# Kernel optimization log

Hardware: AMD Instinct MI355X
Metric: run time of the kernel (lower is better)

The kernel has to match this reference:

```python
import jax, jax.numpy as jnp
import numpy as np

EPS = 1e-5
INV_SQRT2 = 0.7071067811865476

def _rmsnorm(x, w):
    rms = jnp.sqrt(jnp.sum(x * x, axis=-1) / x.shape[-1] + EPS)
    return x / rms[..., None] * w

def _gelu(x):
    # exact erf-based GELU as in the torch module
    return x * (1.0 + jax.scipy.special.erf(x * INV_SQRT2)) * 0.5

def setup_inputs() -> dict:
    key = jax.random.key(0)
    ks = jax.random.split(key, 8)
    B, S, D, DFF = 4, 2048, 1024, 4096
    s = 0.02  # realistic init scale keeps softmax non-degenerate
    return {
        "x": jax.random.normal(ks[0], (B, S, D), jnp.float32),
        "ln1": jax.random.uniform(ks[1], (D,), jnp.float32),
        "ln2": jax.random.uniform(ks[2], (D,), jnp.float32),
        "ffn1": jax.random.normal(ks[3], (DFF, D), jnp.float32) * s,
        "ffn2": jax.random.normal(ks[4], (D, DFF), jnp.float32) * s,
        "k_proj": jax.random.normal(ks[5], (D, D), jnp.float32) * s,
        "q_proj": jax.random.normal(ks[6], (D, D), jnp.float32) * s,
        "v_proj": jax.random.normal(ks[7], (D, D), jnp.float32) * s,
        "out_proj": jax.random.normal(jax.random.fold_in(key, 99), (D, D), jnp.float32) * s,
    }

def reference(x, ln1, ln2, ffn1, ffn2, k_proj, q_proj, v_proj, out_proj):
    S = x.shape[1]
    d_k = x.shape[-1]
    # --- attention branch (single-head, as in source) ---
    h = _rmsnorm(x, ln1)
    Q = h @ q_proj.T  # [B,S,D]
    K = h @ k_proj.T
    V = h @ v_proj.T
    scores = jnp.einsum('bqd,bkd->bqk', Q, K) / jnp.sqrt(jnp.float32(d_k))
    attn = jax.nn.softmax(scores, axis=-1)
    # source: softmax first, then zero out strict-upper (future) entries, renormalize
    causal = jnp.tril(jnp.ones((S, S), jnp.float32))
    attn = attn * causal
    attn = attn / jnp.sum(attn, axis=-1, keepdims=True)
    mh = jnp.einsum('bqk,bkd->bqd', attn, V) @ out_proj
    y = x + mh
    # --- FFN branch: NOTE source feeds RMSNorm2(x), not y ---
    h2 = _rmsnorm(x, ln2)
    ff = _gelu(h2 @ ffn1.T) @ ffn2.T
    return y + ff
```

## Files before the change

### kernel.cpp

```cpp
#include <hip/hip_runtime.h>
#include <math.h>

typedef __bf16 bf16_t;
typedef __bf16 bf16x8 __attribute__((ext_vector_type(8)));
typedef float f32x4 __attribute__((ext_vector_type(4)));

#define LDS16(g, l) __builtin_amdgcn_global_load_lds( \
    (__attribute__((address_space(1))) void*)(g),     \
    (__attribute__((address_space(3))) void*)(l), 16, 0, 0)

__global__ __launch_bounds__(256) void prep_kernel(
    const float* __restrict__ qp, const float* __restrict__ kp,
    const float* __restrict__ vp, const float* __restrict__ f1,
    const float* __restrict__ f2, const float* __restrict__ op,
    const float* __restrict__ x, const float* __restrict__ ln1,
    bf16_t* __restrict__ qkvb, bf16_t* __restrict__ f1b,
    bf16_t* __restrict__ f2b, bf16_t* __restrict__ opT,
    bf16_t* __restrict__ h1)
{
    __shared__ float tile[32][33];
    __shared__ float red[4];
    int bid = blockIdx.x;
    int t = threadIdx.x;
    if (bid < 11264) {
        size_t i = ((size_t)bid * 256 + t) * 4;
        const float* src;
        bf16_t* dst;
        if (i < 3145728) {
            if (i < 1048576)      { src = qp + i;             dst = qkvb + i; }
            else if (i < 2097152) { src = kp + (i - 1048576); dst = qkvb + i; }
            else                  { src = vp + (i - 2097152); dst = qkvb + i; }
        } else if (i < 7340032) { src = f1 + (i - 3145728); dst = f1b + (i - 3145728); }
        else                    { src = f2 + (i - 7340032); dst = f2b + (i - 7340032); }
        float4 v = *(const float4*)src;
        dst[0] = (bf16_t)v.x; dst[1] = (bf16_t)v.y;
        dst[2] = (bf16_t)v.z; dst[3] = (bf16_t)v.w;
    } else if (bid < 12288) {
        int b2 = bid - 11264;
        int c0 = (b2 & 31) * 32, r0 = (b2 >> 5) * 32;
        int tx = t & 31, ty = t >> 5;
#pragma unroll
        for (int i = 0; i < 32; i += 8)
            tile[ty + i][tx] = op[(size_t)(r0 + ty + i) * 1024 + c0 + tx];
        __syncthreads();
#pragma unroll
        for (int i = 0; i < 32; i += 8)
            opT[(size_t)(c0 + ty + i) * 1024 + r0 + tx] = (bf16_t)tile[tx][ty + i];
    } else {
        int row = bid - 12288;
        float4 xv = ((const float4*)(x + (size_t)row * 1024))[t];
        float ss = xv.x * xv.x + xv.y * xv.y + xv.z * xv.z + xv.w * xv.w;
#pragma unroll
        for (int o = 32; o > 0; o >>= 1) ss += __shfl_xor(ss, o, 64);
        if ((t & 63) == 0) red[t >> 6] = ss;
        __syncthreads();
        ss = red[0] + red[1] + red[2] + red[3];
        float rinv = rsqrtf(ss * (1.0f / 1024.0f) + 1e-5f);
        float4 wv = ((const float4*)ln1)[t];
        bf16_t* hp = h1 + (size_t)row * 1024 + t * 4;
        hp[0] = (bf16_t)(xv.x * rinv * wv.x);
        hp[1] = (bf16_t)(xv.y * rinv * wv.y);
        hp[2] = (bf16_t)(xv.z * rinv * wv.z);
        hp[3] = (bf16_t)(xv.w * rinv * wv.w);
    }
}

__global__ __launch_bounds__(256) void rmsnorm_kernel(
    const float* __restrict__ x, const float* __restrict__ w,
    bf16_t* __restrict__ h)
{
    int row = blockIdx.x;
    int t = threadIdx.x;
    float4 xv = ((const float4*)(x + (size_t)row * 1024))[t];
    float ss = xv.x * xv.x + xv.y * xv.y + xv.z * xv.z + xv.w * xv.w;
#pragma unroll
    for (int o = 32; o > 0; o >>= 1) ss += __shfl_xor(ss, o, 64);
    __shared__ float red[4];
    if ((t & 63) == 0) red[t >> 6] = ss;
    __syncthreads();
    ss = red[0] + red[1] + red[2] + red[3];
    float rinv = rsqrtf(ss * (1.0f / 1024.0f) + 1e-5f);
    float4 wv = ((const float4*)w)[t];
    bf16_t* hp = h + (size_t)row * 1024 + t * 4;
    hp[0] = (bf16_t)(xv.x * rinv * wv.x);
    hp[1] = (bf16_t)(xv.y * rinv * wv.y);
    hp[2] = (bf16_t)(xv.z * rinv * wv.z);
    hp[3] = (bf16_t)(xv.w * rinv * wv.w);
}

__global__ __launch_bounds__(256) void transpose_bf16(
    const bf16_t* __restrict__ in, bf16_t* __restrict__ out,
    int rows, int ldin, long long sIn, long long sOut)
{
    __shared__ bf16_t tile[32][33];
    int b = blockIdx.z;
    const bf16_t* ip = in + (long long)b * sIn;
    bf16_t* op = out + (long long)b * sOut;
    int c0 = blockIdx.x * 32, r0 = blockIdx.y * 32;
    int tx = threadIdx.x & 31, ty = threadIdx.x >> 5;
#pragma unroll
    for (int i = 0; i < 32; i += 8)
        tile[ty + i][tx] = ip[(size_t)(r0 + ty + i) * ldin + c0 + tx];
    __syncthreads();
#pragma unroll
    for (int i = 0; i < 32; i += 8)
        op[(size_t)(c0 + ty + i) * rows + r0 + tx] = tile[tx][ty + i];
}

__global__ __launch_bounds__(256) void causal_softmax_kernel(bf16_t* __restrict__ SP)
{
    const int S = 2048;
    int q = blockIdx.x, b = blockIdx.y;
    bf16_t* row = SP + ((size_t)b * S + q) * S;
    int t = threadIdx.x;
    int j0 = t * 8;
    int Jstore = ((q >> 7) + 1) << 7;

    float v[8];
    if (j0 + 7 <= q) {
        bf16x8 xv = *(const bf16x8*)(row + j0);
#pragma unroll
        for (int i = 0; i < 8; i++) v[i] = (float)xv[i];
    } else if (j0 <= q) {
#pragma unroll
        for (int i = 0; i < 8; i++)
            v[i] = (j0 + i <= q) ? (float)row[j0 + i] : -1e30f;
    } else {
#pragma unroll
        for (int i = 0; i < 8; i++) v[i] = -1e30f;
    }

    float mx = v[0];
#pragma unroll
    for (int i = 1; i < 8; i++) mx = fmaxf(mx, v[i]);
#pragma unroll
    for (int o = 32; o > 0; o >>= 1) mx = fmaxf(mx, __shfl_xor(mx, o, 64));
    __shared__ float sm[4], ssum[4];
    if ((t & 63) == 0) sm[t >> 6] = mx;
    __syncthreads();
    mx = fmaxf(fmaxf(sm[0], sm[1]), fmaxf(sm[2], sm[3]));

    float e[8];
    float sum = 0.f;
#pragma unroll
    for (int i = 0; i < 8; i++) {
        e[i] = (v[i] > -1e29f) ? expf(v[i] - mx) : 0.f;
        sum += e[i];
    }
#pragma unroll
    for (int o = 32; o > 0; o >>= 1) sum += __shfl_xor(sum, o, 64);
    if ((t & 63) == 0) ssum[t >> 6] = sum;
    __syncthreads();
    sum = ssum[0] + ssum[1] + ssum[2] + ssum[3];
    float r = 1.0f / sum;

    if (j0 < Jstore) {
        bf16x8 ov;
#pragma unroll
        for (int i = 0; i < 8; i++) ov[i] = (bf16_t)(e[i] * r);
        *(bf16x8*)(row + j0) = ov;
    }
}

template <int EPI, bool TRI, bool CKLOOP>
__global__ __launch_bounds__(256) void gemm_bt(
    const bf16_t* __restrict__ A, int lda, const bf16_t* __restrict__ B, int ldb,
    void* Cv, int ldc, const float* R,
    int K, int Nt, long long sA, long long sB, long long sC, float scale)
{
    int bz = blockIdx.z;
    int bm, bn;
    if (TRI) {
        int i = blockIdx.x;
        bm = (int)((sqrtf(8.0f * i + 1.0f) - 1.0f) * 0.5f);
        while ((bm + 1) * (bm + 2) / 2 <= i) bm++;
        while (bm * (bm + 1) / 2 > i) bm--;
        bn = i - bm * (bm + 1) / 2;
    } else {
        int id = blockIdx.x;
        int xcd = id & 7, p = id >> 3;
        int cn = Nt >> 3;
        bn = xcd * cn + p % cn;
        bm = p / cn;
    }

    __shared__ __align__(16) bf16_t At[128 * 64];
    __shared__ __align__(16) bf16_t Bt[128 * 64];
    int t = threadIdx.x;
    int w = t >> 6, l = t & 63;
    int wm = w >> 1, wn = w & 1;
    int lane_m = l & 15, quad = l >> 4;

    const bf16_t* Ag = A + (long long)bz * sA + (size_t)(bm * 128) * lda;
    const bf16_t* Bg = B + (long long)bz * sB + (size_t)(bn * 128) * ldb;

    int Keff = K;
    if (CKLOOP) {
        int kk = (bm + 1) * 128;
        if (kk < K) Keff = kk;
    }

    f32x4 acc[4][4] = {};

    int rb = w * 8 + (l >> 3);
    int g0 = ((l & 7) ^ ((l >> 3) & 7)) * 8;
    const bf16_t* a0[4];
    const bf16_t* b0[4];
#pragma unroll
    for (int j = 0; j < 4; j++) {
        size_t ro = (size_t)(rb + 32 * j);
        a0[j] = Ag + ro * lda + g0;
        b0[j] = Bg + ro * ldb + g0;
    }

    int s0 = (quad ^ (lane_m & 7)) * 8;
    int s1 = ((4 + quad) ^ (lane_m & 7)) * 8;

    for (int kt = 0; kt < Keff; kt += 64) {
        __syncthreads();
#pragma unroll
        for (int j = 0; j < 4; j++) {
            LDS16(a0[j] + kt, At + (size_t)w * 512 + j * 2048);
            LDS16(b0[j] + kt, Bt + (size_t)w * 512 + j * 2048);
        }
        __syncthreads();

#pragma unroll
        for (int h = 0; h < 2; h++) {
            int sh = h ? s1 : s0;
            bf16x8 af[4], bfr[4];
#pragma unroll
            for (int mi = 0; mi < 4; mi++)
                af[mi] = *(const bf16x8*)(At + (wm * 64 + mi * 16 + lane_m) * 64 + sh);
#pragma unroll
            for (int ni = 0; ni < 4; ni++)
                bfr[ni] = *(const bf16x8*)(Bt + (wn * 64 + ni * 16 + lane_m) * 64 + sh);
#pragma unroll
            for (int mi = 0; mi < 4; mi++)
#pragma unroll
                for (int ni = 0; ni < 4; ni++)
                    acc[mi][ni] = __builtin_amdgcn_mfma_f32_16x16x32_bf16(
                        af[mi], bfr[ni], acc[mi][ni], 0, 0, 0);
        }
    }

    long long cbase = (long long)bz * sC;
#pragma unroll
    for (int mi = 0; mi < 4; mi++) {
#pragma unroll
        for (int r = 0; r < 4; r++) {
            int row = bm * 128 + wm * 64 + mi * 16 + quad * 4 + r;
#pragma unroll
            for (int ni = 0; ni < 4; ni++) {
                int col = bn * 128 + wn * 64 + ni * 16 + lane_m;
                float v = acc[mi][ni][r];
                size_t idx = (size_t)(cbase + (long long)row * ldc + col);
                if (EPI == 0) {
                    ((bf16_t*)Cv)[idx] = (bf16_t)(v * scale);
                } else if (EPI == 1) {
                    float g = 0.5f * v * (1.0f + erff(v * 0.70710678118654752f));
                    ((bf16_t*)Cv)[idx] = (bf16_t)g;
                } else {
                    float rv = R[(size_t)row * ldc + col];
                    ((float*)Cv)[idx] = v + rv;
                }
            }
        }
    }
}

extern "C" void kernel_launch(void* const* d_in, const int* in_sizes, int n_in,
                              void* d_out, int out_size, void* d_ws, size_t ws_size,
                              hipStream_t stream)
{
    (void)in_sizes; (void)n_in; (void)out_size;
    const float* x    = (const float*)d_in[0];
    const float* ln1  = (const float*)d_in[1];
    const float* ln2  = (const float*)d_in[2];
    const float* ffn1 = (const float*)d_in[3];
    const float* ffn2 = (const float*)d_in[4];
    const float* kp   = (const float*)d_in[5];
    const float* qp   = (const float*)d_in[6];
    const float* vp   = (const float*)d_in[7];
    const float* op   = (const float*)d_in[8];
    float* out = (float*)d_out;

    const size_t MiB = 1048576;
    char* ws = (char*)d_ws;
    bf16_t* qkvb = (bf16_t*)(ws + 0 * MiB);
    bf16_t* opT  = (bf16_t*)(ws + 6 * MiB);
    bf16_t* f1b  = (bf16_t*)(ws + 8 * MiB);
    bf16_t* f2b  = (bf16_t*)(ws + 16 * MiB);
    bf16_t* h1   = (bf16_t*)(ws + 24 * MiB);
    bf16_t* VT   = (bf16_t*)(ws + 24 * MiB);
    bf16_t* h2   = (bf16_t*)(ws + 24 * MiB);
    bf16_t* QKVb = (bf16_t*)(ws + 40 * MiB);
    bf16_t* AV   = (bf16_t*)(ws + 40 * MiB);
    bf16_t* G    = (bf16_t*)(ws + 40 * MiB);
    bf16_t* SP   = (bf16_t*)d_out;
    bool bigws = ws_size >= 104 * MiB;

    dim3 blk(256);

    prep_kernel<<<dim3(20480), blk, 0, stream>>>(
        qp, kp, vp, ffn1, ffn2, op, x, ln1, qkvb, f1b, f2b, opT, h1);

    gemm_bt<0, false, false><<<dim3(1536), blk, 0, stream>>>(
        h1, 1024, qkvb, 1024, QKVb, 3072, nullptr, 1024, 24, 0, 0, 0, 1.0f);

    gemm_bt<0, true, false><<<dim3(136, 1, 4), blk, 0, stream>>>(
        QKVb, 3072, QKVb + 1024, 3072, SP, 2048, nullptr, 1024, 16,
        (long long)2048 * 3072, (long long)2048 * 3072, (long long)2048 * 2048,
        1.0f / 32.0f);

    transpose_bf16<<<dim3(32, 64, 4), blk, 0, stream>>>(
        QKVb + 2048, VT, 2048, 3072,
        (long long)2048 * 3072, (long long)1024 * 2048);

    causal_softmax_kernel<<<dim3(2048, 4), blk, 0, stream>>>(SP);

    gemm_bt<0, false, true><<<dim3(128, 1, 4), blk, 0, stream>>>(
        SP, 2048, VT, 2048, AV, 1024, nullptr, 2048, 8,
        (long long)2048 * 2048, (long long)1024 * 2048, (long long)2048 * 1024,
        1.0f);

    gemm_bt<2, false, false><<<dim3(512), blk, 0, stream>>>(
        AV, 1024, opT, 1024, out, 1024, x, 1024, 8, 0, 0, 0, 1.0f);

    rmsnorm_kernel<<<dim3(8192), blk, 0, stream>>>(x, ln2, h2);

    if (bigws) {
        gemm_bt<1, false, false><<<dim3(2048), blk, 0, stream>>>(
            h2, 1024, f1b, 1024, G, 4096, nullptr, 1024, 32, 0, 0, 0, 1.0f);
        gemm_bt<2, false, false><<<dim3(512), blk, 0, stream>>>(
            G, 4096, f2b, 4096, out, 1024, out, 4096, 8, 0, 0, 0, 1.0f);
    } else {
        for (int half = 0; half < 2; half++) {
            gemm_bt<1, false, false><<<dim3(1024), blk, 0, stream>>>(
                h2, 1024, f1b + (size_t)half * 2048 * 1024, 1024, G, 2048,
                nullptr, 1024, 16, 0, 0, 0, 1.0f);
            gemm_bt<2, false, false><<<dim3(512), blk, 0, stream>>>(
                G, 2048, f2b + half * 2048, 4096, out, 1024, out,
                2048, 8, 0, 0, 0, 1.0f);
        }
    }
}
```

Before: 545.9 us.

## Partition GEMM tiles by M across XCDs and split-K the FFN2 GEMM with atomics

Changes the default tile-to-XCD mapping so each XCD owns a contiguous band of M rows instead of N columns. This targets L2 reuse of the A operand within each XCD. The per-batch attention GEMM keeps the old N-partition through a new template flag. The FFN2 GEMM is split across K into two slices that atomically accumulate into the output, which already holds x plus attention, doubling its block count for better occupancy. The atomics add memory traffic and make the float summation order nondeterministic.

```diff
diff --git a/kernel.cpp b/kernel.cpp
--- a/kernel.cpp
+++ b/kernel.cpp
@@ -162,11 +162,11 @@
     }
 }
 
-template <int EPI, bool TRI, bool CKLOOP>
+template <int EPI, bool TRI, bool CKLOOP, bool NPART, bool SPLITK>
 __global__ __launch_bounds__(256) void gemm_bt(
     const bf16_t* __restrict__ A, int lda, const bf16_t* __restrict__ B, int ldb,
     void* Cv, int ldc, const float* R,
-    int K, int Nt, long long sA, long long sB, long long sC, float scale)
+    int K, int Pt, long long sA, long long sB, long long sC, float scale)
 {
     int bz = blockIdx.z;
     int bm, bn;
@@ -176,12 +176,18 @@
         while ((bm + 1) * (bm + 2) / 2 <= i) bm++;
         while (bm * (bm + 1) / 2 > i) bm--;
         bn = i - bm * (bm + 1) / 2;
+    } else if (NPART) {
+        int id = blockIdx.x;
+        int xcd = id & 7, p = id >> 3;
+        int cn = Pt >> 3;
+        bn = xcd * cn + p % cn;
+        bm = p / cn;
     } else {
         int id = blockIdx.x;
         int xcd = id & 7, p = id >> 3;
-        int cn = Nt >> 3;
-        bn = xcd * cn + p % cn;
-        bm = p / cn;
+        int cm = Pt >> 3;
+        bm = xcd * cm + p % cm;
+        bn = p / cm;
     }
 
     __shared__ __align__(16) bf16_t At[128 * 64];
@@ -194,10 +200,15 @@
     const bf16_t* Ag = A + (long long)bz * sA + (size_t)(bm * 128) * lda;
     const bf16_t* Bg = B + (long long)bz * sB + (size_t)(bn * 128) * ldb;
 
-    int Keff = K;
+    int kbeg = 0, kend = K;
+    if (SPLITK) {
+        int Ksl = K >> 1;
+        kbeg = blockIdx.y * Ksl;
+        kend = kbeg + Ksl;
+    }
     if (CKLOOP) {
         int kk = (bm + 1) * 128;
-        if (kk < K) Keff = kk;
+        if (kk < kend) kend = kk;
     }
 
     f32x4 acc[4][4] = {};
@@ -216,7 +227,7 @@
     int s0 = (quad ^ (lane_m & 7)) * 8;
     int s1 = ((4 + quad) ^ (lane_m & 7)) * 8;
 
-    for (int kt = 0; kt < Keff; kt += 64) {
+    for (int kt = kbeg; kt < kend; kt += 64) {
         __syncthreads();
 #pragma unroll
         for (int j = 0; j < 4; j++) {
@@ -260,9 +271,11 @@
                 } else if (EPI == 1) {
                     float g = 0.5f * v * (1.0f + erff(v * 0.70710678118654752f));
                     ((bf16_t*)Cv)[idx] = (bf16_t)g;
-                } else {
+                } else if (EPI == 2) {
                     float rv = R[(size_t)row * ldc + col];
                     ((float*)Cv)[idx] = v + rv;
+                } else {
+                    atomicAdd((float*)Cv + idx, v);
                 }
             }
         }
@@ -305,10 +318,10 @@
     prep_kernel<<<dim3(20480), blk, 0, stream>>>(
         qp, kp, vp, ffn1, ffn2, op, x, ln1, qkvb, f1b, f2b, opT, h1);
 
-    gemm_bt<0, false, false><<<dim3(1536), blk, 0, stream>>>(
-        h1, 1024, qkvb, 1024, QKVb, 3072, nullptr, 1024, 24, 0, 0, 0, 1.0f);
-
-    gemm_bt<0, true, false><<<dim3(136, 1, 4), blk, 0, stream>>>(
+    gemm_bt<0, false, false, false, false><<<dim3(1536), blk, 0, stream>>>(
+        h1, 1024, qkvb, 1024, QKVb, 3072, nullptr, 1024, 64, 0, 0, 0, 1.0f);
+
+    gemm_bt<0, true, false, false, false><<<dim3(136, 1, 4), blk, 0, stream>>>(
         QKVb, 3072, QKVb + 1024, 3072, SP, 2048, nullptr, 1024, 16,
         (long long)2048 * 3072, (long long)2048 * 3072, (long long)2048 * 2048,
         1.0f / 32.0f);
@@ -319,29 +332,29 @@
 
     causal_softmax_kernel<<<dim3(2048, 4), blk, 0, stream>>>(SP);
 
-    gemm_bt<0, false, true><<<dim3(128, 1, 4), blk, 0, stream>>>(
+    gemm_bt<0, false, true, true, false><<<dim3(128, 1, 4), blk, 0, stream>>>(
         SP, 2048, VT, 2048, AV, 1024, nullptr, 2048, 8,
         (long long)2048 * 2048, (long long)1024 * 2048, (long long)2048 * 1024,
         1.0f);
 
-    gemm_bt<2, false, false><<<dim3(512), blk, 0, stream>>>(
-        AV, 1024, opT, 1024, out, 1024, x, 1024, 8, 0, 0, 0, 1.0f);
+    gemm_bt<2, false, false, false, false><<<dim3(512), blk, 0, stream>>>(
+        AV, 1024, opT, 1024, out, 1024, x, 1024, 64, 0, 0, 0, 1.0f);
 
     rmsnorm_kernel<<<dim3(8192), blk, 0, stream>>>(x, ln2, h2);
 
     if (bigws) {
-        gemm_bt<1, false, false><<<dim3(2048), blk, 0, stream>>>(
-            h2, 1024, f1b, 1024, G, 4096, nullptr, 1024, 32, 0, 0, 0, 1.0f);
-        gemm_bt<2, false, false><<<dim3(512), blk, 0, stream>>>(
-            G, 4096, f2b, 4096, out, 1024, out, 4096, 8, 0, 0, 0, 1.0f);
+        gemm_bt<1, false, false, false, false><<<dim3(2048), blk, 0, stream>>>(
+            h2, 1024, f1b, 1024, G, 4096, nullptr, 1024, 64, 0, 0, 0, 1.0f);
+        gemm_bt<3, false, false, false, true><<<dim3(512, 2), blk, 0, stream>>>(
+            G, 4096, f2b, 4096, out, 1024, nullptr, 4096, 64, 0, 0, 0, 1.0f);
     } else {
         for (int half = 0; half < 2; half++) {
-            gemm_bt<1, false, false><<<dim3(1024), blk, 0, stream>>>(
+            gemm_bt<1, false, false, false, false><<<dim3(1024), blk, 0, stream>>>(
                 h2, 1024, f1b + (size_t)half * 2048 * 1024, 1024, G, 2048,
-                nullptr, 1024, 16, 0, 0, 0, 1.0f);
-            gemm_bt<2, false, false><<<dim3(512), blk, 0, stream>>>(
-                G, 2048, f2b + half * 2048, 4096, out, 1024, out,
-                2048, 8, 0, 0, 0, 1.0f);
+                nullptr, 1024, 64, 0, 0, 0, 1.0f);
+            gemm_bt<3, false, false, false, false><<<dim3(512), blk, 0, stream>>>(
+                G, 2048, f2b + half * 2048, 4096, out, 1024, nullptr,
+                2048, 64, 0, 0, 0, 1.0f);
         }
     }
 }
```

Result: slower. 558.2 us (+2.3%).
